# Performance work log

Measured on AMD Instinct MI355X. Metric: run time of the kernel, lower is better.

## Reference

```python
import jax, jax.numpy as jnp
import numpy as np

EMB = 32      # emb_size = input_size // 2
IN = 64       # input_size
H = 128       # hidden_size
OUT = 256     # output_size (byte vocab)
TEMP = 1e-3   # Decoder_lstm.temperature


def _bytes(x):
    # x: [N] nonneg int32 -> [N, 4] big-endian bytes (vectorized get_bytes_2d)
    shifts = jnp.array([24, 16, 8, 0], dtype=x.dtype)
    return (x[:, None] >> shifts) & 0xFF


def _embed4(tables, byts):
    # tables: [4, 256, EMB]; byts: [N, 4] -> [N, 4*EMB] (concat of 4 gathers)
    return jnp.concatenate([tables[i][byts[:, i]] for i in range(4)], axis=-1)


def _encoder(x, W, b):
    # Encoder: sigmoid(Linear(4*EMB -> EMB))
    return jax.nn.sigmoid(x @ W.T + b)


def _lstm(xs, h0, c0, W_ih, W_hh, b_ih, b_hh):
    # xs: [S, B, IN]; PyTorch gate order i, f, g, o
    def step(carry, x_t):
        h, c = carry
        g = x_t @ W_ih.T + b_ih + h @ W_hh.T + b_hh  # [B, 4H]
        i, f, gg, o = jnp.split(g, 4, axis=-1)
        c = jax.nn.sigmoid(f) * c + jax.nn.sigmoid(i) * jnp.tanh(gg)
        h = jax.nn.sigmoid(o) * jnp.tanh(c)
        return (h, c), None
    (hf, cf), _ = jax.lax.scan(step, (h0, c0), xs)
    return hf, cf


def reference(inp, h0, c0, pc_emb, addr_emb, enc_W, enc_b, W_ih, W_hh, b_ih, b_hh, dec_W, dec_b, fc1_W, fc1_b, fc2_W, fc2_b):
    b, s, _ = inp.shape
    pc = inp[:, :, 0].reshape(-1)
    ad = inp[:, :, 1].reshape(-1)
    # byte decomposition + embedding gather + TimeDistributed encoder MLP
    pc_e = _encoder(_embed4(pc_emb, _bytes(pc)), enc_W, enc_b).reshape(b, s, EMB)
    ad_e = _encoder(_embed4(addr_emb, _bytes(ad)), enc_W, enc_b).reshape(b, s, EMB)
    emb = jnp.concatenate([pc_e, ad_e], axis=-1)  # [b, s, IN]
    # deterministic surrogate for KDE sample mean (expected value of 200 KDE draws)
    dist = jnp.mean(emb, axis=1)  # [b, IN]
    hf, _ = _lstm(jnp.swapaxes(emb, 0, 1), h0[0], c0[0], W_ih, W_hh, b_ih, b_hh)
    h_n = hf[None]  # [1, b, H] == hidden_cell[0]
    # Decoder_lstm: 4 parallel linears + low-temperature softmax
    logits = jnp.einsum('xbh,koh->kxbo', h_n, dec_W) + dec_b[:, None, None, :]  # [4,1,b,OUT]
    probs = jax.nn.softmax(logits / TEMP, axis=-1)
    # get_freq_rec: probs @ embedding tables, encoder MLP, concat dist, small MLP
    be = jnp.einsum('kxbo,koe->xbke', probs, addr_emb).reshape(1, b, 4 * EMB)
    fe = _encoder(be, enc_W, enc_b)[0]  # [b, EMB]
    fr_in = jnp.concatenate([fe, dist], axis=-1)  # [b, 3*EMB]
    fr = jax.nn.sigmoid(jax.nn.relu(fr_in @ fc1_W.T + fc1_b) @ fc2_W.T + fc2_b)
    return probs, logits, fr[:, 0], fr[:, 1]


def setup_inputs() -> dict:
    ks = jax.random.split(jax.random.key(0), 18)
    B, S = 64, 2048
    g = lambda k, shp: 0.1 * jax.random.normal(k, shp, dtype=jnp.float32)
    return {
        'inp': jax.random.randint(ks[0], (B, S, 2), 0, 2147483647, dtype=jnp.int32),
        'h0': g(ks[1], (1, B, H)),
        'c0': g(ks[2], (1, B, H)),
        'pc_emb': g(ks[3], (4, 256, EMB)),
        'addr_emb': g(ks[4], (4, 256, EMB)),
        'enc_W': g(ks[5], (EMB, 4 * EMB)),
        'enc_b': g(ks[6], (EMB,)),
        'W_ih': g(ks[7], (4 * H, IN)),
        'W_hh': g(ks[8], (4 * H, H)),
        'b_ih': g(ks[9], (4 * H,)),
        'b_hh': g(ks[10], (4 * H,)),
        'dec_W': g(ks[11], (4, OUT, H)),
        'dec_b': g(ks[12], (4, OUT)),
        'fc1_W': g(ks[13], (10, 3 * EMB)),
        'fc1_b': g(ks[14], (10,)),
        'fc2_W': g(ks[15], (2, 10)),
        'fc2_b': g(ks[16], (2,)),
    }
```

## Files before the change

### kernel.cpp

```cpp
#include <hip/hip_runtime.h>
#include <math.h>
#include <stdint.h>

#define EMBS 32
#define INS 64
#define HS 128
#define OUTS 256
#define BS 64
#define SS 2048

typedef _Float16 half2v __attribute__((ext_vector_type(2)));

static constexpr size_t WS_DIST  = (size_t)BS * SS * INS;
static constexpr size_t WS_HFIN  = WS_DIST + (size_t)BS * INS;
static constexpr size_t WS_XW    = WS_HFIN + (size_t)BS * HS;
static constexpr size_t WS_SMALL = WS_XW;
static constexpr size_t WS_BIG   = WS_XW + (size_t)BS * SS * 256;

__device__ __forceinline__ float fexp2(float x) {
#if __has_builtin(__builtin_amdgcn_exp2f)
    return __builtin_amdgcn_exp2f(x);
#else
    return exp2f(x);
#endif
}
__device__ __forceinline__ float frcp(float x) {
#if __has_builtin(__builtin_amdgcn_rcpf)
    return __builtin_amdgcn_rcpf(x);
#else
    return 1.f / x;
#endif
}
__device__ __forceinline__ float sigm(float x)  { return frcp(1.f + fexp2(-1.44269504f * x)); }
__device__ __forceinline__ float ftanh(float x) { return 1.f - 2.f * frcp(1.f + fexp2(2.88539008f * x)); }

__device__ __forceinline__ float fdot2f(half2v a, half2v b, float c) {
#if __has_builtin(__builtin_amdgcn_fdot2)
    return __builtin_amdgcn_fdot2(a, b, c, false);
#else
    return c + (float)a.x * (float)b.x + (float)a.y * (float)b.y;
#endif
}

__device__ __forceinline__ half2v pack2(float a, float b) {
    half2v r; r.x = (_Float16)a; r.y = (_Float16)b; return r;
}

__device__ __forceinline__ void gate_map(int tid, int& u, bool& lo, int& g0, int& g1) {
    int l = tid & 63;
    u = ((tid >> 6) << 5) + (l & 31);
    lo = (l < 32);
    g0 = lo ? u : 128 + u;
    g1 = lo ? 256 + u : 384 + u;
}

__global__ __launch_bounds__(256) void k_embed(
    const int* __restrict__ inp, const float* __restrict__ pc_emb,
    const float* __restrict__ ad_emb, const float* __restrict__ encW,
    const float* __restrict__ encB, float* __restrict__ emb)
{
    int idx = blockIdx.x * 256 + threadIdx.x;
    int b = idx >> 11, t = idx & 2047;
    size_t base = (size_t)b * SS + t;
    int2 pa = ((const int2*)inp)[base];
    float* outp = emb + base * INS;

    float in[128];
    #pragma unroll
    for (int st = 0; st < 2; st++) {
        int v = (st == 0) ? pa.x : pa.y;
        const float* tbl = (st == 0) ? pc_emb : ad_emb;
        #pragma unroll
        for (int i = 0; i < 4; i++) {
            int by = (v >> (24 - 8 * i)) & 255;
            const float4* row = (const float4*)(tbl + ((size_t)i * 256 + by) * EMBS);
            #pragma unroll
            for (int k = 0; k < 8; k++) {
                float4 f = row[k];
                in[i * 32 + k * 4 + 0] = f.x;
                in[i * 32 + k * 4 + 1] = f.y;
                in[i * 32 + k * 4 + 2] = f.z;
                in[i * 32 + k * 4 + 3] = f.w;
            }
        }
        for (int e = 0; e < EMBS; e++) {
            const float* w = encW + e * 128;
            float acc = encB[e];
            #pragma unroll
            for (int k = 0; k < 128; k++) acc += in[k] * w[k];
            outp[st * EMBS + e] = sigm(acc);
        }
    }
}

__global__ __launch_bounds__(256) void k_dist(const float* __restrict__ emb,
                                              float* __restrict__ dist)
{
    int b = blockIdx.x;
    int j = threadIdx.x & 63;
    int grp = threadIdx.x >> 6;
    float s = 0.f;
    for (int t = grp; t < SS; t += 4) s += emb[((size_t)b * SS + t) * INS + j];
    __shared__ float red[4][64];
    red[grp][j] = s;
    __syncthreads();
    if (grp == 0)
        dist[b * 64 + j] = (red[0][j] + red[1][j] + red[2][j] + red[3][j]) * (1.f / SS);
}

#define XW_ROWS 64
__global__ __launch_bounds__(256) void k_xw(
    const float* __restrict__ emb, const float* __restrict__ Wih,
    const float* __restrict__ bih, const float* __restrict__ bhh,
    half2v* __restrict__ xwv)
{
    int tid = threadIdx.x;
    size_t r0 = (size_t)blockIdx.x * XW_ROWS;
    int u, g0, g1; bool lo;
    gate_map(tid, u, lo, g0, g1);

    half2v wa[32], wb[32];
    const float* pa_ = Wih + (size_t)g0 * INS;
    const float* pb_ = Wih + (size_t)g1 * INS;
    #pragma unroll
    for (int i = 0; i < 32; i++) {
        wa[i] = pack2(pa_[2 * i], pa_[2 * i + 1]);
        wb[i] = pack2(pb_[2 * i], pb_[2 * i + 1]);
    }
    float ba = bih[g0] + bhh[g0], bb = bih[g1] + bhh[g1];

    __shared__ alignas(16) half2v xsh[XW_ROWS * 32];
    const float4* src = (const float4*)(emb + r0 * INS);
    #pragma unroll
    for (int k = 0; k < 4; k++) {
        int fi = k * 256 + tid;
        float4 v = src[fi];
        xsh[fi * 2]     = pack2(v.x, v.y);
        xsh[fi * 2 + 1] = pack2(v.z, v.w);
    }
    __syncthreads();

    #pragma unroll 2
    for (int r = 0; r < XW_ROWS; r++) {
        const half2v* xr = &xsh[r * 32];
        float a0 = 0.f, a1 = 0.f, b0 = 0.f, b1 = 0.f;
        #pragma unroll
        for (int i = 0; i < 32; i += 2) {
            half2v x0 = xr[i], x1 = xr[i + 1];
            a0 = fdot2f(x0, wa[i], a0);
            a1 = fdot2f(x1, wa[i + 1], a1);
            b0 = fdot2f(x0, wb[i], b0);
            b1 = fdot2f(x1, wb[i + 1], b1);
        }
        xwv[(r0 + r) * 256 + tid] = pack2(ba + a0 + a1, bb + b0 + b1);
    }
}

__global__ __launch_bounds__(256, 1) void k_lstm6(
    const half2v* __restrict__ xw, const float* __restrict__ h0,
    const float* __restrict__ c0, const float* __restrict__ Whh,
    float* __restrict__ hfin)
{
    int b = blockIdx.x;
    int tid = threadIdx.x;
    int u, g0_, g1_; bool lo;
    gate_map(tid, u, lo, g0_, g1_);
    int koff = lo ? 0 : 64;
    int kv   = lo ? 0 : 32;

    half2v wI[32], wF[32], wG[32], wO[32];
    {
        const float* rI = Whh + (size_t)(u)       * HS + koff;
        const float* rF = Whh + (size_t)(128 + u) * HS + koff;
        const float* rG = Whh + (size_t)(256 + u) * HS + koff;
        const float* rO = Whh + (size_t)(384 + u) * HS + koff;
        #pragma unroll
        for (int i = 0; i < 32; i++) {
            wI[i] = pack2(rI[2 * i], rI[2 * i + 1]);
            wF[i] = pack2(rF[2 * i], rF[2 * i + 1]);
            wG[i] = pack2(rG[2 * i], rG[2 * i + 1]);
            wO[i] = pack2(rO[2 * i], rO[2 * i + 1]);
        }
    }

    __shared__ alignas(16) _Float16 hsh[2][HS];
    float c = 0.f, h = 0.f;
    if (!lo) c = c0[b * HS + u];
    if (tid < 128) hsh[0][tid] = (_Float16)h0[b * HS + tid];
    __syncthreads();

    const half2v* xwrow = xw + (size_t)b * SS * 256 + tid;
    half2v xb0 = xwrow[0];
    half2v xb1 = xwrow[256];
    half2v xb2 = xwrow[512];
    half2v xb3 = xwrow[768];

#define LSTEP(XB, RB, TN)                                                      \
    {                                                                          \
        const half2v* hb = (const half2v*)hsh[RB] + kv;                        \
        half2v hr[32];                                                         \
        _Pragma("unroll")                                                      \
        for (int j_ = 0; j_ < 32; j_++) hr[j_] = hb[j_];                       \
        float pI = 0.f, pF = 0.f, pG = 0.f, pO = 0.f;                          \
        _Pragma("unroll")                                                      \
        for (int j_ = 0; j_ < 32; j_++) {                                      \
            half2v hv = hr[j_];                                                \
            pI = fdot2f(hv, wI[j_], pI);                                       \
            pF = fdot2f(hv, wF[j_], pF);                                       \
            pG = fdot2f(hv, wG[j_], pG);                                       \
            pO = fdot2f(hv, wO[j_], pO);                                       \
        }                                                                      \
                \
        float r1 = __shfl_xor(lo ? pF : pI, 32, 64); \
        float r2 = __shfl_xor(lo ? pO : pG, 32, 64); \
        float pre0 = (lo ? pI : pF) + r1 + (float)XB.x;                        \
        float pre1 = (lo ? pG : pO) + r2 + (float)XB.y;                        \
        float act0 = sigm(pre0);                            \
        float act1 = lo ? ftanh(pre1) : sigm(pre1);         \
        float pig = __shfl_xor(act0 * act1, 32, 64);      \
        if (!lo) {                                                             \
            c = __builtin_fmaf(act0, c, pig);                                  \
            h = act1 * ftanh(c);                                               \
            hsh[RB ^ 1][u] = (_Float16)h;                                      \
        }                                                                      \
        {                                                                      \
            int tn_ = (TN) < SS ? (TN) : (SS - 1);                             \
            XB = xwrow[(size_t)tn_ * 256];                                     \
        }                                                                      \
        asm volatile("s_waitcnt lgkmcnt(0)" ::: "memory");                     \
        __builtin_amdgcn_s_barrier();                                          \
        __builtin_amdgcn_sched_barrier(0);                                     \
    }

    for (int t = 0; t < SS; t += 4) {
        LSTEP(xb0, 0, t + 4)
        LSTEP(xb1, 1, t + 5)
        LSTEP(xb2, 0, t + 6)
        LSTEP(xb3, 1, t + 7)
    }
#undef LSTEP

    if (!lo) hfin[b * HS + u] = h;
}

__global__ __launch_bounds__(256, 1) void k_lstm_fb(
    const float* __restrict__ emb, const float* __restrict__ h0,
    const float* __restrict__ c0, const float* __restrict__ Wih,
    const float* __restrict__ Whh, const float* __restrict__ bih,
    const float* __restrict__ bhh, float* __restrict__ hfin)
{
    int b = blockIdx.x;
    int tid = threadIdx.x;

    half2v wih[2][32], whh[2][64];
    #pragma unroll
    for (int g = 0; g < 2; g++) {
        int gg = tid + g * 256;
        const float* wr = Wih + (size_t)gg * INS;
        #pragma unroll
        for (int i = 0; i < 32; i++) wih[g][i] = pack2(wr[2 * i], wr[2 * i + 1]);
        const float* hr = Whh + (size_t)gg * HS;
        #pragma unroll
        for (int i = 0; i < 64; i++) whh[g][i] = pack2(hr[2 * i], hr[2 * i + 1]);
    }
    float bias0 = bih[tid] + bhh[tid];
    float bias1 = bih[tid + 256] + bhh[tid + 256];

    __shared__ alignas(16) half2v xh[96];
    __shared__ float f_act[128], o_act[128];
    __shared__ float xf[64], hf[128];

    float c = 0.f, h = 0.f;
    if (tid < 128) c = c0[b * HS + tid];

    const float* xrow = emb + (size_t)b * SS * INS;
    if (tid < 64) xf[tid] = xrow[tid];
    if (tid < 128) hf[tid] = h0[b * HS + tid];
    __syncthreads();
    if (tid < 32) xh[tid] = pack2(xf[2 * tid], xf[2 * tid + 1]);
    else if (tid < 96) { int uu = tid - 32; xh[tid] = pack2(hf[2 * uu], hf[2 * uu + 1]); }
    __syncthreads();

    for (int t = 0; t < SS; t++) {
        float xn = 0.f;
        if (tid >= 128 && tid < 192 && t + 1 < SS) xn = xrow[(size_t)(t + 1) * INS + (tid - 128)];

        float a0a = 0.f, a0b = 0.f, a1a = 0.f, a1b = 0.f;
        #pragma unroll
        for (int i = 0; i < 32; i += 2) {
            half2v x0 = xh[i], x1 = xh[i + 1];
            a0a = fdot2f(x0, wih[0][i], a0a);
            a0b = fdot2f(x1, wih[0][i + 1], a0b);
            a1a = fdot2f(x0, wih[1][i], a1a);
            a1b = fdot2f(x1, wih[1][i + 1], a1b);
        }
        #pragma unroll
        for (int i = 0; i < 64; i += 2) {
            half2v h0v = xh[32 + i], h1v = xh[32 + i + 1];
            a0a = fdot2f(h0v, whh[0][i], a0a);
            a0b = fdot2f(h1v, whh[0][i + 1], a0b);
            a1a = fdot2f(h0v, whh[1][i], a1a);
            a1b = fdot2f(h1v, whh[1][i + 1], a1b);
        }
        float a0 = bias0 + a0a + a0b;
        float a1 = bias1 + a1a + a1b;

        float iact = 0.f, gact = 0.f;
        if (tid < 128) { iact = sigm(a0); gact = ftanh(a1); }
        else           { f_act[tid - 128] = sigm(a0); o_act[tid - 128] = sigm(a1); }
        __syncthreads();

        if (tid < 128) {
            c = f_act[tid] * c + iact * gact;
            h = o_act[tid] * ftanh(c);
            hf[tid] = h;
        } else if (tid < 192) {
            xf[tid - 128] = xn;
        }
        __syncthreads();

        if (tid < 32) xh[tid] = pack2(xf[2 * tid], xf[2 * tid + 1]);
        else if (tid < 96) { int uu = tid - 32; xh[tid] = pack2(hf[2 * uu], hf[2 * uu + 1]); }
        __syncthreads();
    }
    if (tid < 128) hfin[b * HS + tid] = h;
}

__global__ __launch_bounds__(256) void k_head(
    const float* __restrict__ hfin, const float* __restrict__ decW,
    const float* __restrict__ decB, const float* __restrict__ ad_emb,
    const float* __restrict__ encW, const float* __restrict__ encB,
    const float* __restrict__ dist, const float* __restrict__ fc1W,
    const float* __restrict__ fc1b, const float* __restrict__ fc2W,
    const float* __restrict__ fc2b, float* __restrict__ outp)
{
    int b = blockIdx.x;
    int tid = threadIdx.x;
    __shared__ float hsh[128];
    __shared__ float logit_s[4][256];
    __shared__ float probs_s[4][256];
    __shared__ float be_s[128];
    __shared__ float fe_dist[96];
    __shared__ float fr1[10];

    if (tid < 128) hsh[tid] = hfin[b * HS + tid];
    __syncthreads();

    #pragma unroll
    for (int k = 0; k < 4; k++) {
        const float* w = decW + ((size_t)k * OUTS + tid) * HS;
        float acc = decB[k * OUTS + tid];
        #pragma unroll 8
        for (int hh = 0; hh < HS; hh++) acc += hsh[hh] * w[hh];
        logit_s[k][tid] = acc;
        outp[65536 + k * 16384 + b * 256 + tid] = acc;
    }
    __syncthreads();

    {
        int k = tid >> 6, lane = tid & 63;
        float v0 = logit_s[k][lane],       v1 = logit_s[k][lane + 64];
        float v2 = logit_s[k][lane + 128], v3 = logit_s[k][lane + 192];
        float m = fmaxf(fmaxf(v0, v1), fmaxf(v2, v3));
        for (int off = 32; off; off >>= 1) m = fmaxf(m, __shfl_xor(m, off, 64));
        float e0 = fexp2((v0 - m) * 1442.695041f), e1 = fexp2((v1 - m) * 1442.695041f);
        float e2 = fexp2((v2 - m) * 1442.695041f), e3 = fexp2((v3 - m) * 1442.695041f);
        float s = e0 + e1 + e2 + e3;
        for (int off = 32; off; off >>= 1) s += __shfl_xor(s, off, 64);
        float inv = 1.f / s;
        float p0 = e0 * inv, p1 = e1 * inv, p2 = e2 * inv, p3 = e3 * inv;
        probs_s[k][lane] = p0;        probs_s[k][lane + 64] = p1;
        probs_s[k][lane + 128] = p2;  probs_s[k][lane + 192] = p3;
        outp[k * 16384 + b * 256 + lane] = p0;
        outp[k * 16384 + b * 256 + lane + 64] = p1;
        outp[k * 16384 + b * 256 + lane + 128] = p2;
        outp[k * 16384 + b * 256 + lane + 192] = p3;
    }
    __syncthreads();

    if (tid < 128) {
        int k = tid >> 5, e = tid & 31;
        const float* te = ad_emb + (size_t)k * OUTS * EMBS + e;
        float acc = 0.f;
        #pragma unroll 8
        for (int o = 0; o < OUTS; o++) acc += probs_s[k][o] * te[o * EMBS];
        be_s[tid] = acc;
    }
    __syncthreads();

    if (tid < 32) {
        const float* w = encW + tid * 128;
        float acc = encB[tid];
        #pragma unroll 8
        for (int kk = 0; kk < 128; kk++) acc += be_s[kk] * w[kk];
        fe_dist[tid] = sigm(acc);
    } else if (tid < 96) {
        fe_dist[tid] = dist[b * 64 + (tid - 32)];
    }
    __syncthreads();

    if (tid < 10) {
        float acc = fc1b[tid];
        for (int kk = 0; kk < 96; kk++) acc += fe_dist[kk] * fc1W[tid * 96 + kk];
        fr1[tid] = fmaxf(acc, 0.f);
    }
    __syncthreads();

    if (tid < 2) {
        float acc = fc2b[tid];
        for (int kk = 0; kk < 10; kk++) acc += fr1[kk] * fc2W[tid * 10 + kk];
        outp[131072 + tid * 64 + b] = sigm(acc);
    }
}

extern "C" void kernel_launch(void* const* d_in, const int* in_sizes, int n_in,
                              void* d_out, int out_size, void* d_ws, size_t ws_size,
                              hipStream_t stream)
{
    const int*   inp    = (const int*)d_in[0];
    const float* h0     = (const float*)d_in[1];
    const float* c0     = (const float*)d_in[2];
    const float* pc_emb = (const float*)d_in[3];
    const float* ad_emb = (const float*)d_in[4];
    const float* encW   = (const float*)d_in[5];
    const float* encB   = (const float*)d_in[6];
    const float* Wih    = (const float*)d_in[7];
    const float* Whh    = (const float*)d_in[8];
    const float* bih    = (const float*)d_in[9];
    const float* bhh    = (const float*)d_in[10];
    const float* decW   = (const float*)d_in[11];
    const float* decB   = (const float*)d_in[12];
    const float* fc1W   = (const float*)d_in[13];
    const float* fc1b   = (const float*)d_in[14];
    const float* fc2W   = (const float*)d_in[15];
    const float* fc2b   = (const float*)d_in[16];

    if (ws_size < WS_SMALL * 4ull) return;

    float* ws   = (float*)d_ws;
    float* emb  = ws;
    float* dist = ws + WS_DIST;
    float* hfin = ws + WS_HFIN;
    float* outp = (float*)d_out;
    bool big = (ws_size >= WS_BIG * 4ull);

    hipLaunchKernelGGL(k_embed, dim3(512), dim3(256), 0, stream,
                       inp, pc_emb, ad_emb, encW, encB, emb);
    hipLaunchKernelGGL(k_dist, dim3(64), dim3(256), 0, stream, emb, dist);
    if (big) {
        half2v* xwv = (half2v*)(ws + WS_XW);
        hipLaunchKernelGGL(k_xw, dim3(BS * SS / XW_ROWS), dim3(256), 0, stream,
                           emb, Wih, bih, bhh, xwv);
        hipLaunchKernelGGL(k_lstm6, dim3(64), dim3(256), 0, stream,
                           xwv, h0, c0, Whh, hfin);
    } else {
        hipLaunchKernelGGL(k_lstm_fb, dim3(64), dim3(256), 0, stream,
                           emb, h0, c0, Wih, Whh, bih, bhh, hfin);
    }
    hipLaunchKernelGGL(k_head, dim3(64), dim3(256), 0, stream,
                       hfin, decW, decB, ad_emb, encW, encB, dist,
                       fc1W, fc1b, fc2W, fc2b, outp);
}
```

Before: 1.497 ms.

## Precompute per-byte encoder projections and vectorize LDS reads in LSTM and head

```diff
diff --git a/kernel.cpp b/kernel.cpp
--- a/kernel.cpp
+++ b/kernel.cpp
@@ -10,10 +10,15 @@
 #define SS 2048
 
 typedef _Float16 half2v __attribute__((ext_vector_type(2)));
+typedef _Float16 half8  __attribute__((ext_vector_type(8)));
+typedef float f32x4 __attribute__((ext_vector_type(4)));
+
+typedef union { half8 v; half2v p[4]; } h8u;
 
 static constexpr size_t WS_DIST  = (size_t)BS * SS * INS;
 static constexpr size_t WS_HFIN  = WS_DIST + (size_t)BS * INS;
-static constexpr size_t WS_XW    = WS_HFIN + (size_t)BS * HS;
+static constexpr size_t WS_P     = WS_HFIN + (size_t)BS * HS;
+static constexpr size_t WS_XW    = WS_P + 2ull * 4 * 256 * 32;
 static constexpr size_t WS_SMALL = WS_XW;
 static constexpr size_t WS_BIG   = WS_XW + (size_t)BS * SS * 256;
 
@@ -54,42 +59,53 @@
     g1 = lo ? 256 + u : 384 + u;
 }
 
-__global__ __launch_bounds__(256) void k_embed(
-    const int* __restrict__ inp, const float* __restrict__ pc_emb,
-    const float* __restrict__ ad_emb, const float* __restrict__ encW,
-    const float* __restrict__ encB, float* __restrict__ emb)
+__global__ __launch_bounds__(256) void k_pre(
+    const float* __restrict__ pc_emb, const float* __restrict__ ad_emb,
+    const float* __restrict__ encW, const float* __restrict__ encB,
+    float* __restrict__ P)
 {
     int idx = blockIdx.x * 256 + threadIdx.x;
-    int b = idx >> 11, t = idx & 2047;
-    size_t base = (size_t)b * SS + t;
+    int e = idx & 31, by = (idx >> 5) & 255, i = (idx >> 13) & 3, st = idx >> 15;
+    const float* tbl = (st ? ad_emb : pc_emb) + ((size_t)i * 256 + by) * EMBS;
+    const float* w = encW + e * 128 + i * 32;
+    float acc = (i == 0) ? encB[e] : 0.f;
+    #pragma unroll
+    for (int k = 0; k < 32; k++) acc += w[k] * tbl[k];
+    P[idx] = acc;
+}
+
+__global__ __launch_bounds__(256) void k_embed2(
+    const int* __restrict__ inp, const float* __restrict__ P,
+    float* __restrict__ emb)
+{
+    int idx = blockIdx.x * 256 + threadIdx.x;
+    size_t base = (size_t)idx;
     int2 pa = ((const int2*)inp)[base];
     float* outp = emb + base * INS;
 
-    float in[128];
     #pragma unroll
     for (int st = 0; st < 2; st++) {
-        int v = (st == 0) ? pa.x : pa.y;
-        const float* tbl = (st == 0) ? pc_emb : ad_emb;
+        int v = st ? pa.y : pa.x;
+        const float* Ps = P + st * 32768;
+        float acc[32];
         #pragma unroll
         for (int i = 0; i < 4; i++) {
             int by = (v >> (24 - 8 * i)) & 255;
-            const float4* row = (const float4*)(tbl + ((size_t)i * 256 + by) * EMBS);
+            const float4* row = (const float4*)(Ps + ((size_t)i * 256 + by) * 32);
             #pragma unroll
             for (int k = 0; k < 8; k++) {
                 float4 f = row[k];
-                in[i * 32 + k * 4 + 0] = f.x;
-                in[i * 32 + k * 4 + 1] = f.y;
-                in[i * 32 + k * 4 + 2] = f.z;
-                in[i * 32 + k * 4 + 3] = f.w;
+                if (i == 0) {
+                    acc[k * 4 + 0] = f.x; acc[k * 4 + 1] = f.y;
+                    acc[k * 4 + 2] = f.z; acc[k * 4 + 3] = f.w;
+                } else {
+                    acc[k * 4 + 0] += f.x; acc[k * 4 + 1] += f.y;
+                    acc[k * 4 + 2] += f.z; acc[k * 4 + 3] += f.w;
+                }
             }
         }
-        for (int e = 0; e < EMBS; e++) {
-            const float* w = encW + e * 128;
-            float acc = encB[e];
-            #pragma unroll
-            for (int k = 0; k < 128; k++) acc += in[k] * w[k];
-            outp[st * EMBS + e] = sigm(acc);
-        }
+        #pragma unroll
+        for (int e = 0; e < 32; e++) outp[st * 32 + e] = sigm(acc[e]);
     }
 }
 
@@ -142,11 +158,14 @@
 
     #pragma unroll 2
     for (int r = 0; r < XW_ROWS; r++) {
-        const half2v* xr = &xsh[r * 32];
+        const half8* xr8 = (const half8*)&xsh[r * 32];
+        h8u x8[8];
+        #pragma unroll
+        for (int k = 0; k < 8; k++) x8[k].v = xr8[k];
         float a0 = 0.f, a1 = 0.f, b0 = 0.f, b1 = 0.f;
         #pragma unroll
         for (int i = 0; i < 32; i += 2) {
-            half2v x0 = xr[i], x1 = xr[i + 1];
+            half2v x0 = x8[i >> 2].p[i & 3], x1 = x8[(i + 1) >> 2].p[(i + 1) & 3];
             a0 = fdot2f(x0, wa[i], a0);
             a1 = fdot2f(x1, wa[i + 1], a1);
             b0 = fdot2f(x0, wb[i], b0);
@@ -156,7 +175,7 @@
     }
 }
 
-__global__ __launch_bounds__(256, 1) void k_lstm6(
+__global__ __launch_bounds__(256, 1) void k_lstm8(
     const half2v* __restrict__ xw, const float* __restrict__ h0,
     const float* __restrict__ c0, const float* __restrict__ Whh,
     float* __restrict__ hfin)
@@ -166,7 +185,6 @@
     int u, g0_, g1_; bool lo;
     gate_map(tid, u, lo, g0_, g1_);
     int koff = lo ? 0 : 64;
-    int kv   = lo ? 0 : 32;
 
     half2v wI[32], wF[32], wG[32], wO[32];
     {
@@ -197,22 +215,32 @@
 
 #define LSTEP(XB, RB, TN)                                                      \
     {                                                                          \
-        const half2v* hb = (const half2v*)hsh[RB] + kv;                        \
-        half2v hr[32];                                                         \
+        const half8* hb8 = (const half8*)(&hsh[RB][0] + koff);                 \
+        h8u h8[8];                                                             \
         _Pragma("unroll")                                                      \
-        for (int j_ = 0; j_ < 32; j_++) hr[j_] = hb[j_];                       \
-        float pI = 0.f, pF = 0.f, pG = 0.f, pO = 0.f;                          \
+        for (int k_ = 0; k_ < 8; k_++) h8[k_].v = hb8[k_];        \
+        float pIa = 0.f, pFa = 0.f, pGa = 0.f, pOa = 0.f;                      \
+        float pIb = 0.f, pFb = 0.f, pGb = 0.f, pOb = 0.f;                      \
         _Pragma("unroll")                                                      \
-        for (int j_ = 0; j_ < 32; j_++) {                                      \
-            half2v hv = hr[j_];                                                \
-            pI = fdot2f(hv, wI[j_], pI);                                       \
-            pF = fdot2f(hv, wF[j_], pF);                                       \
-            pG = fdot2f(hv, wG[j_], pG);                                       \
-            pO = fdot2f(hv, wO[j_], pO);                                       \
+        for (int j_ = 0; j_ < 16; j_++) {                                      \
+            half2v hv = h8[j_ >> 2].p[j_ & 3];                                 \
+            pIa = fdot2f(hv, wI[j_], pIa);                                     \
+            pFa = fdot2f(hv, wF[j_], pFa);                                     \
+            pGa = fdot2f(hv, wG[j_], pGa);                                     \
+            pOa = fdot2f(hv, wO[j_], pOa);                                     \
         }                                                                      \
-                \
-        float r1 = __shfl_xor(lo ? pF : pI, 32, 64); \
-        float r2 = __shfl_xor(lo ? pO : pG, 32, 64); \
+        _Pragma("unroll")                                                      \
+        for (int j_ = 16; j_ < 32; j_++) {                                     \
+            half2v hv = h8[j_ >> 2].p[j_ & 3];                                 \
+            pIb = fdot2f(hv, wI[j_], pIb);                                     \
+            pFb = fdot2f(hv, wF[j_], pFb);                                     \
+            pGb = fdot2f(hv, wG[j_], pGb);                                     \
+            pOb = fdot2f(hv, wO[j_], pOb);                                     \
+        }                                                                      \
+        float pI = pIa + pIb, pF = pFa + pFb;                                  \
+        float pG = pGa + pGb, pO = pOa + pOb;                                  \
+        float r1 = __shfl_xor(lo ? pF : pI, 32, 64);                           \
+        float r2 = __shfl_xor(lo ? pO : pG, 32, 64);                           \
         float pre0 = (lo ? pI : pF) + r1 + (float)XB.x;                        \
         float pre1 = (lo ? pG : pO) + r2 + (float)XB.y;                        \
         float act0 = sigm(pre0);                            \
@@ -336,7 +364,7 @@
 {
     int b = blockIdx.x;
     int tid = threadIdx.x;
-    __shared__ float hsh[128];
+    __shared__ alignas(16) float hsh[128];
     __shared__ float logit_s[4][256];
     __shared__ float probs_s[4][256];
     __shared__ float be_s[128];
@@ -346,14 +374,27 @@
     if (tid < 128) hsh[tid] = hfin[b * HS + tid];
     __syncthreads();
 
-    #pragma unroll
-    for (int k = 0; k < 4; k++) {
-        const float* w = decW + ((size_t)k * OUTS + tid) * HS;
-        float acc = decB[k * OUTS + tid];
-        #pragma unroll 8
-        for (int hh = 0; hh < HS; hh++) acc += hsh[hh] * w[hh];
-        logit_s[k][tid] = acc;
-        outp[65536 + k * 16384 + b * 256 + tid] = acc;
+    {
+        f32x4 hv[32];
+        const f32x4* h4 = (const f32x4*)hsh;
+        #pragma unroll
+        for (int j = 0; j < 32; j++) hv[j] = h4[j];
+        #pragma unroll
+        for (int k = 0; k < 4; k++) {
+            const float4* w4 = (const float4*)(decW + ((size_t)k * OUTS + tid) * HS);
+            float a0 = decB[k * OUTS + tid], a1 = 0.f;
+            #pragma unroll
+            for (int j = 0; j < 32; j++) {
+                float4 wv = w4[j];
+                a0 = __builtin_fmaf(hv[j][0], wv.x, a0);
+                a1 = __builtin_fmaf(hv[j][1], wv.y, a1);
+                a0 = __builtin_fmaf(hv[j][2], wv.z, a0);
+                a1 = __builtin_fmaf(hv[j][3], wv.w, a1);
+            }
+            float acc = a0 + a1;
+            logit_s[k][tid] = acc;
+            outp[65536 + k * 16384 + b * 256 + tid] = acc;
+        }
     }
     __syncthreads();
 
@@ -441,17 +482,20 @@
     float* emb  = ws;
     float* dist = ws + WS_DIST;
     float* hfin = ws + WS_HFIN;
+    float* P    = ws + WS_P;
     float* outp = (float*)d_out;
     bool big = (ws_size >= WS_BIG * 4ull);
 
-    hipLaunchKernelGGL(k_embed, dim3(512), dim3(256), 0, stream,
-                       inp, pc_emb, ad_emb, encW, encB, emb);
+    hipLaunchKernelGGL(k_pre, dim3(256), dim3(256), 0, stream,
+                       pc_emb, ad_emb, encW, encB, P);
+    hipLaunchKernelGGL(k_embed2, dim3(512), dim3(256), 0, stream,
+                       inp, P, emb);
     hipLaunchKernelGGL(k_dist, dim3(64), dim3(256), 0, stream, emb, dist);
     if (big) {
         half2v* xwv = (half2v*)(ws + WS_XW);
         hipLaunchKernelGGL(k_xw, dim3(BS * SS / XW_ROWS), dim3(256), 0, stream,
                            emb, Wih, bih, bhh, xwv);
-        hipLaunchKernelGGL(k_lstm6, dim3(64), dim3(256), 0, stream,
+        hipLaunchKernelGGL(k_lstm8, dim3(64), dim3(256), 0, stream,
                            xwv, h0, c0, Whh, hfin);
     } else {
         hipLaunchKernelGGL(k_lstm_fb, dim3(64), dim3(256), 0, stream,
```

Measured after the change: 1.424 ms. 1.05x faster.
